# Kernel optimization log

Measured on AMD Instinct MI355X. Metric: run time of the kernel, lower is better.

Reference implementation:

```python
import jax, jax.numpy as jnp
import numpy as np

N_TP = 4  # number of heterogeneous agent types (experts)


def _mlp(x, w1, b1, w2, b2, w3, b3):
    h = jax.nn.relu(x @ w1 + b1)
    h = jax.nn.relu(h @ w2 + b2)
    return h @ w3 + b3


def setup_inputs() -> dict:
    key = jax.random.key(0)
    ks = jax.random.split(key, 12)
    T, A, D, H, NA = 2048, 128, 64, 64, 16
    s = 0.05
    return {
        "obs": jax.random.normal(ks[0], (T, A, D), dtype=jnp.float32),
        "hete_pick": jax.random.randint(ks[1], (T, A), 0, N_TP, dtype=jnp.int64),
        "gp_sel_summary": jax.random.uniform(ks[2], (T, N_TP), dtype=jnp.float32),
        "W1": jax.random.normal(ks[3], (N_TP, D + N_TP, H), dtype=jnp.float32) * s,
        "b1": jnp.zeros((N_TP, H), jnp.float32),
        "W2": jax.random.normal(ks[4], (N_TP, H, H), dtype=jnp.float32) * s,
        "b2": jnp.zeros((N_TP, H), jnp.float32),
        "W3": jax.random.normal(ks[5], (N_TP, H, NA), dtype=jnp.float32) * s,
        "b3": jnp.zeros((N_TP, NA), jnp.float32),
        "cW1": jax.random.normal(ks[6], (D + N_TP, H), dtype=jnp.float32) * s,
        "cb1": jnp.zeros((H,), jnp.float32),
        "cW2": jax.random.normal(ks[7], (H, H), dtype=jnp.float32) * s,
        "cb2": jnp.zeros((H,), jnp.float32),
        "cW3": jax.random.normal(ks[8], (H, 1), dtype=jnp.float32) * s,
        "cb3": jnp.zeros((1,), jnp.float32),
    }


def reference(obs, hete_pick, gp_sel_summary, W1, b1, W2, b2, W3, b3,
              cW1, cb1, cW2, cb2, cW3, cb3):
    T, A, D = obs.shape
    n_tp = W1.shape[0]
    # hete_info_obs: broadcast group-selection summary over agents, concat to obs
    hete_info = jnp.broadcast_to(gp_sel_summary[:, None, :], (T, A, n_tp))
    x = jnp.concatenate([obs, hete_info.astype(obs.dtype)], axis=-1)  # [T,A,D+n_tp]
    xf = x.reshape(T * A, D + n_tp)
    tp = hete_pick.reshape(T * A)
    # per-type dispatch: mask -> sub-net -> scatter back (expressed as masked select)
    logits = jnp.zeros((T * A, W3.shape[-1]), obs.dtype)
    for t in range(n_tp):
        out_t = _mlp(xf, W1[t], b1[t], W2[t], b2[t], W3[t], b3[t])
        logits = jnp.where((tp == t)[:, None], out_t, logits)
    # central critic runs on all agents
    value = _mlp(xf, cW1, cb1, cW2, cb2, cW3, cb3)  # [T*A,1]
    out = jnp.concatenate([logits, value], axis=-1)  # [T*A, n_action+1]
    return out.reshape(T, A, -1)
```

## Files before the change

kernel.cpp:

```cpp
#include <hip/hip_runtime.h>
#include <stdint.h>


typedef float v4f __attribute__((ext_vector_type(4)));
typedef short v8s __attribute__((ext_vector_type(8)));

#define NTOK   262144
#define XS_STR 104
#define HS_STR 136
#define WP2_OFF 30720
#define WP3_OFF 51200

static __device__ __forceinline__ short f2bf(float f) {
    union { float f; uint32_t u; } c; c.f = f;
    uint32_t u = c.u;
    uint32_t r = (u + 0x7FFFu + ((u >> 16) & 1u)) >> 16;
    return (short)r;
}


__global__ void count_kernel(const int* __restrict__ hete, int* __restrict__ hdr) {
    __shared__ int wc[4][4];
    int tid = threadIdx.x, lane = tid & 63, w = tid >> 6;
    int i = blockIdx.x * 256 + tid;
    int e = hete[i];
#pragma unroll
    for (int t = 0; t < 4; t++) {
        unsigned long long m = __ballot(e == t);
        if (lane == 0) wc[w][t] = __popcll(m);
    }
    __syncthreads();
    if (tid < 4) {
        int s = wc[0][tid] + wc[1][tid] + wc[2][tid] + wc[3][tid];
        atomicAdd(&hdr[tid], s);
    }
}

__global__ void prefix_kernel(int* __restrict__ hdr, int* __restrict__ bucket) {
    __shared__ int sa[5], sc[4];
    int tid = threadIdx.x;
    if (tid == 0) {
        int a = 0, ts = 0;
        for (int e = 0; e < 4; e++) {
            int c = hdr[e];
            sc[e] = c;
            sa[e] = a;
            hdr[4 + e]  = a;
            hdr[8 + e]  = a;
            hdr[13 + e] = ts;
            int tiles = (c + 127) >> 7;
            a  += tiles << 7;
            ts += tiles;
        }
        sa[4]   = a;
        hdr[12] = a;
        hdr[17] = ts;
    }
    __syncthreads();
    for (int e = 0; e < 4; e++) {
        int start = sa[e] + sc[e];
        int end   = sa[e + 1];
        for (int i = start + tid; i < end; i += 256) bucket[i] = -1;
    }
}

__global__ void scatter_kernel(const int* __restrict__ hete, int* __restrict__ hdr,
                               int* __restrict__ bucket) {
    __shared__ int wc[4][4], wb[4][4];
    int tid = threadIdx.x, lane = tid & 63, w = tid >> 6;
    int i = blockIdx.x * 256 + tid;
    int e = hete[i];
    unsigned long long lt = (1ull << lane) - 1ull;
    int rank = 0;
#pragma unroll
    for (int t = 0; t < 4; t++) {
        unsigned long long m = __ballot(e == t);
        if (lane == 0) wc[w][t] = __popcll(m);
        if (e == t) rank = __popcll(m & lt);
    }
    __syncthreads();
    if (tid < 4) {
        int t = tid, tot = 0;
#pragma unroll
        for (int ww = 0; ww < 4; ww++) tot += wc[ww][t];
        int base = atomicAdd(&hdr[4 + t], tot);
#pragma unroll
        for (int ww = 0; ww < 4; ww++) { int c = wc[ww][t]; wb[ww][t] = base; base += c; }
    }
    __syncthreads();
    bucket[wb[w][e] + rank] = i;
}


__global__ void prep_kernel(const float* __restrict__ W1, const float* __restrict__ cW1,
                            const float* __restrict__ W2, const float* __restrict__ cW2,
                            const float* __restrict__ W3, const float* __restrict__ cW3,
                            short* __restrict__ wp) {
    int b = blockIdx.x, lane = threadIdx.x;
    int nl = lane & 15, quad = lane >> 4;
    short frag[8];
    if (b < 60) {
        int e = b / 12, rem = b % 12, ks = rem / 4, nt = rem % 4;
        int n = nt * 16 + nl;
#pragma unroll
        for (int j = 0; j < 8; j++) {
            int k = ks * 32 + quad * 8 + j;
            float v = 0.f;
            if (k < 68) v = (e < 4) ? W1[(e * 68 + k) * 64 + n] : cW1[k * 64 + n];
            frag[j] = f2bf(v);
        }
    } else if (b < 100) {
        int u = b - 60, e = u / 8, ks = (u % 8) / 4, nt = u % 4;
        int n = nt * 16 + nl;
#pragma unroll
        for (int j = 0; j < 8; j++) {
            int k = ks * 32 + quad * 8 + j;
            frag[j] = f2bf((e < 4) ? W2[(e * 64 + k) * 64 + n] : cW2[k * 64 + n]);
        }
    } else {
        int u = b - 100;
#pragma unroll
        for (int j = 0; j < 8; j++) {
            int ks = (u < 8) ? (u & 1) : (u - 8);
            int k  = ks * 32 + quad * 8 + j;
            float v;
            if (u < 8) { int ee = u >> 1; v = W3[(ee * 64 + k) * 16 + nl]; }
            else       { v = (nl == 0) ? cW3[k] : 0.f; }
            frag[j] = f2bf(v);
        }
    }
    v8s pk = { frag[0], frag[1], frag[2], frag[3], frag[4], frag[5], frag[6], frag[7] };
    *(v8s*)(wp + (size_t)b * 512 + lane * 8) = pk;
}


__global__ __launch_bounds__(256) void main_kernel(
    const float* __restrict__ obs, const float* __restrict__ gp,
    const int* __restrict__ bucket, const int* __restrict__ hdr,
    const short* __restrict__ wp,
    const float* __restrict__ b1, const float* __restrict__ b2, const float* __restrict__ b3,
    const float* __restrict__ cb1, const float* __restrict__ cb2, const float* __restrict__ cb3,
    float* __restrict__ out)
{
    __shared__ __align__(16) short xs[128 * XS_STR];
    __shared__ __align__(16) short hs[128 * HS_STR];
    __shared__ int tokL[128];

    int b = blockIdx.x;
    int total = hdr[17];
    if (b >= total) return;
    int e = 3;
    if      (b < hdr[14]) e = 0;
    else if (b < hdr[15]) e = 1;
    else if (b < hdr[16]) e = 2;
    int slot0 = hdr[8 + e] + (b - hdr[13 + e]) * 128;

    int tid = threadIdx.x, lane = tid & 63, w = tid >> 6;
    int ml = lane & 15, quad = lane >> 4;

    if (tid < 128) tokL[tid] = bucket[slot0 + tid];

    {
        int r = tid >> 1, hh = tid & 1;
        int tk = bucket[slot0 + r];
        v8s z = { 0, 0, 0, 0, 0, 0, 0, 0 };
        if (tk >= 0) {
            const float4* src = (const float4*)(obs + (size_t)tk * 64 + hh * 32);
#pragma unroll
            for (int t = 0; t < 4; t++) {
                float4 f0 = src[2 * t], f1 = src[2 * t + 1];
                v8s pk = { f2bf(f0.x), f2bf(f0.y), f2bf(f0.z), f2bf(f0.w),
                           f2bf(f1.x), f2bf(f1.y), f2bf(f1.z), f2bf(f1.w) };
                *(v8s*)&xs[r * XS_STR + hh * 32 + t * 8] = pk;
            }
            if (hh) {
                const float* g = gp + (size_t)(tk >> 7) * 4;
                v8s pg = { f2bf(g[0]), f2bf(g[1]), f2bf(g[2]), f2bf(g[3]), 0, 0, 0, 0 };
                *(v8s*)&xs[r * XS_STR + 64] = pg;
                *(v8s*)&xs[r * XS_STR + 72] = z;
                *(v8s*)&xs[r * XS_STR + 80] = z;
                *(v8s*)&xs[r * XS_STR + 88] = z;
            }
        } else {
#pragma unroll
            for (int t = 0; t < 4; t++) *(v8s*)&xs[r * XS_STR + hh * 32 + t * 8] = z;
            if (hh) {
                *(v8s*)&xs[r * XS_STR + 64] = z;
                *(v8s*)&xs[r * XS_STR + 72] = z;
                *(v8s*)&xs[r * XS_STR + 80] = z;
                *(v8s*)&xs[r * XS_STR + 88] = z;
            }
        }
    }
    __syncthreads();

    v4f accE[8], accC[8];
#pragma unroll
    for (int m = 0; m < 8; m++) { accE[m] = (v4f){0,0,0,0}; accC[m] = (v4f){0,0,0,0}; }
#pragma unroll
    for (int ks = 0; ks < 3; ks++) {
        v8s bE = *(const v8s*)(wp + (size_t)((e * 3 + ks) * 4 + w) * 512 + lane * 8);
        v8s bC = *(const v8s*)(wp + (size_t)((12 + ks) * 4 + w) * 512 + lane * 8);
#pragma unroll
        for (int m = 0; m < 8; m++) {
            v8s a = *(const v8s*)&xs[(m * 16 + ml) * XS_STR + ks * 32 + quad * 8];
            accE[m] = __builtin_amdgcn_mfma_f32_16x16x32_bf16(a, bE, accE[m], 0, 0, 0);
            accC[m] = __builtin_amdgcn_mfma_f32_16x16x32_bf16(a, bC, accC[m], 0, 0, 0);
        }
    }
    {
        float bE1 = b1[e * 64 + w * 16 + ml], bC1 = cb1[w * 16 + ml];
#pragma unroll
        for (int m = 0; m < 8; m++)
#pragma unroll
            for (int rr = 0; rr < 4; rr++) {
                int row = m * 16 + quad * 4 + rr;
                hs[row * HS_STR + w * 16 + ml]      = f2bf(fmaxf(accE[m][rr] + bE1, 0.f));
                hs[row * HS_STR + 64 + w * 16 + ml] = f2bf(fmaxf(accC[m][rr] + bC1, 0.f));
            }
    }
    __syncthreads();

    v4f acc2E[8], acc2C[8];
#pragma unroll
    for (int m = 0; m < 8; m++) { acc2E[m] = (v4f){0,0,0,0}; acc2C[m] = (v4f){0,0,0,0}; }
#pragma unroll
    for (int ks = 0; ks < 2; ks++) {
        v8s bE = *(const v8s*)(wp + WP2_OFF + (size_t)((e * 2 + ks) * 4 + w) * 512 + lane * 8);
        v8s bC = *(const v8s*)(wp + WP2_OFF + (size_t)((8 + ks) * 4 + w) * 512 + lane * 8);
#pragma unroll
        for (int m = 0; m < 8; m++) {
            v8s aE = *(const v8s*)&hs[(m * 16 + ml) * HS_STR + ks * 32 + quad * 8];
            v8s aC = *(const v8s*)&hs[(m * 16 + ml) * HS_STR + 64 + ks * 32 + quad * 8];
            acc2E[m] = __builtin_amdgcn_mfma_f32_16x16x32_bf16(aE, bE, acc2E[m], 0, 0, 0);
            acc2C[m] = __builtin_amdgcn_mfma_f32_16x16x32_bf16(aC, bC, acc2C[m], 0, 0, 0);
        }
    }
    __syncthreads();
    {
        float bE2 = b2[e * 64 + w * 16 + ml], bC2 = cb2[w * 16 + ml];
#pragma unroll
        for (int m = 0; m < 8; m++)
#pragma unroll
            for (int rr = 0; rr < 4; rr++) {
                int row = m * 16 + quad * 4 + rr;
                hs[row * HS_STR + w * 16 + ml]      = f2bf(fmaxf(acc2E[m][rr] + bE2, 0.f));
                hs[row * HS_STR + 64 + w * 16 + ml] = f2bf(fmaxf(acc2C[m][rr] + bC2, 0.f));
            }
    }
    __syncthreads();

    v4f accL[2], accV[2];
#pragma unroll
    for (int mm = 0; mm < 2; mm++) { accL[mm] = (v4f){0,0,0,0}; accV[mm] = (v4f){0,0,0,0}; }
#pragma unroll
    for (int ks = 0; ks < 2; ks++) {
        v8s bW = *(const v8s*)(wp + WP3_OFF + (size_t)(e * 2 + ks) * 512 + lane * 8);
        v8s bV = *(const v8s*)(wp + WP3_OFF + (size_t)(8 + ks) * 512 + lane * 8);
#pragma unroll
        for (int mm = 0; mm < 2; mm++) {
            v8s aE = *(const v8s*)&hs[((2 * w + mm) * 16 + ml) * HS_STR + ks * 32 + quad * 8];
            v8s aC = *(const v8s*)&hs[((2 * w + mm) * 16 + ml) * HS_STR + 64 + ks * 32 + quad * 8];
            accL[mm] = __builtin_amdgcn_mfma_f32_16x16x32_bf16(aE, bW, accL[mm], 0, 0, 0);
            accV[mm] = __builtin_amdgcn_mfma_f32_16x16x32_bf16(aC, bV, accV[mm], 0, 0, 0);
        }
    }

    {
        float b3v = b3[e * 16 + ml], cb3v = cb3[0];
#pragma unroll
        for (int mm = 0; mm < 2; mm++)
#pragma unroll
            for (int rr = 0; rr < 4; rr++) {
                int row = (2 * w + mm) * 16 + quad * 4 + rr;
                int tk = tokL[row];
                if (tk >= 0) {
                    float* o = out + (size_t)tk * 17;
                    o[ml] = accL[mm][rr] + b3v;
                    if (ml == 0) o[16] = accV[mm][rr] + cb3v;
                }
            }
    }
}


extern "C" void kernel_launch(void* const* d_in, const int* in_sizes, int n_in,
                              void* d_out, int out_size, void* d_ws, size_t ws_size,
                              hipStream_t stream) {
    const float* obs = (const float*)d_in[0];
    const int*  hete = (const int*)d_in[1];
    const float* gp  = (const float*)d_in[2];
    const float* W1  = (const float*)d_in[3];
    const float* b1  = (const float*)d_in[4];
    const float* W2  = (const float*)d_in[5];
    const float* b2  = (const float*)d_in[6];
    const float* W3  = (const float*)d_in[7];
    const float* b3  = (const float*)d_in[8];
    const float* cW1 = (const float*)d_in[9];
    const float* cb1 = (const float*)d_in[10];
    const float* cW2 = (const float*)d_in[11];
    const float* cb2 = (const float*)d_in[12];
    const float* cW3 = (const float*)d_in[13];
    const float* cb3 = (const float*)d_in[14];
    float* out = (float*)d_out;

    int*   hdr    = (int*)d_ws;
    int*   bucket = hdr + 32;
    short* wp     = (short*)(bucket + 262656);

    hipMemsetAsync(hdr, 0, 128, stream);
    count_kernel  <<<1024, 256, 0, stream>>>(hete, hdr);
    prefix_kernel <<<1,    256, 0, stream>>>(hdr, bucket);
    scatter_kernel<<<1024, 256, 0, stream>>>(hete, hdr, bucket);
    prep_kernel   <<<110,   64, 0, stream>>>(W1, cW1, W2, cW2, W3, cW3, wp);
    main_kernel   <<<2051, 256, 0, stream>>>(obs, gp, bucket, hdr, wp,
                                             b1, b2, b3, cb1, cb2, cb3, out);
}
```

Baseline: 194.4 us.

## Replace bucketed expert dispatch with dense all-expert per-wave MLP evaluation

Removes the count, prefix and scatter kernels and the memset, and computes all four expert MLPs plus the critic for every token, selecting each token's logits by its type (the same masked-select form as the reference). Each wave owns 64 tokens, keeps its input fragments in registers, and uses a per-wave swizzled LDS buffer in place of block-wide shared tiles and barriers. The MFMA operand roles are swapped so that weights are the A operand, and occupancy is hinted through launch bounds. This trades about 2.5x more matrix work for removing the launch overhead of the sort kernels, the gather indirection and the block synchronisation.

```diff
diff --git a/kernel.cpp b/kernel.cpp
--- a/kernel.cpp
+++ b/kernel.cpp
@@ -5,9 +5,6 @@
 typedef float v4f __attribute__((ext_vector_type(4)));
 typedef short v8s __attribute__((ext_vector_type(8)));
 
-#define NTOK   262144
-#define XS_STR 104
-#define HS_STR 136
 #define WP2_OFF 30720
 #define WP3_OFF 51200
 
@@ -17,80 +14,9 @@
     uint32_t r = (u + 0x7FFFu + ((u >> 16) & 1u)) >> 16;
     return (short)r;
 }
-
-
-__global__ void count_kernel(const int* __restrict__ hete, int* __restrict__ hdr) {
-    __shared__ int wc[4][4];
-    int tid = threadIdx.x, lane = tid & 63, w = tid >> 6;
-    int i = blockIdx.x * 256 + tid;
-    int e = hete[i];
-#pragma unroll
-    for (int t = 0; t < 4; t++) {
-        unsigned long long m = __ballot(e == t);
-        if (lane == 0) wc[w][t] = __popcll(m);
-    }
-    __syncthreads();
-    if (tid < 4) {
-        int s = wc[0][tid] + wc[1][tid] + wc[2][tid] + wc[3][tid];
-        atomicAdd(&hdr[tid], s);
-    }
-}
-
-__global__ void prefix_kernel(int* __restrict__ hdr, int* __restrict__ bucket) {
-    __shared__ int sa[5], sc[4];
-    int tid = threadIdx.x;
-    if (tid == 0) {
-        int a = 0, ts = 0;
-        for (int e = 0; e < 4; e++) {
-            int c = hdr[e];
-            sc[e] = c;
-            sa[e] = a;
-            hdr[4 + e]  = a;
-            hdr[8 + e]  = a;
-            hdr[13 + e] = ts;
-            int tiles = (c + 127) >> 7;
-            a  += tiles << 7;
-            ts += tiles;
-        }
-        sa[4]   = a;
-        hdr[12] = a;
-        hdr[17] = ts;
-    }
-    __syncthreads();
-    for (int e = 0; e < 4; e++) {
-        int start = sa[e] + sc[e];
-        int end   = sa[e + 1];
-        for (int i = start + tid; i < end; i += 256) bucket[i] = -1;
-    }
-}
-
-__global__ void scatter_kernel(const int* __restrict__ hete, int* __restrict__ hdr,
-                               int* __restrict__ bucket) {
-    __shared__ int wc[4][4], wb[4][4];
-    int tid = threadIdx.x, lane = tid & 63, w = tid >> 6;
-    int i = blockIdx.x * 256 + tid;
-    int e = hete[i];
-    unsigned long long lt = (1ull << lane) - 1ull;
-    int rank = 0;
-#pragma unroll
-    for (int t = 0; t < 4; t++) {
-        unsigned long long m = __ballot(e == t);
-        if (lane == 0) wc[w][t] = __popcll(m);
-        if (e == t) rank = __popcll(m & lt);
-    }
-    __syncthreads();
-    if (tid < 4) {
-        int t = tid, tot = 0;
-#pragma unroll
-        for (int ww = 0; ww < 4; ww++) tot += wc[ww][t];
-        int base = atomicAdd(&hdr[4 + t], tot);
-#pragma unroll
-        for (int ww = 0; ww < 4; ww++) { int c = wc[ww][t]; wb[ww][t] = base; base += c; }
-    }
-    __syncthreads();
-    bucket[wb[w][e] + rank] = i;
-}
-
+static __device__ __forceinline__ uint32_t pk2(float a, float b) {
+    return (uint32_t)(uint16_t)f2bf(a) | ((uint32_t)(uint16_t)f2bf(b) << 16);
+}
 
 __global__ void prep_kernel(const float* __restrict__ W1, const float* __restrict__ cW1,
                             const float* __restrict__ W2, const float* __restrict__ cW2,
@@ -134,152 +60,158 @@
 }
 
 
-__global__ __launch_bounds__(256) void main_kernel(
+__global__ __launch_bounds__(256, 3) void main_kernel(
     const float* __restrict__ obs, const float* __restrict__ gp,
-    const int* __restrict__ bucket, const int* __restrict__ hdr,
-    const short* __restrict__ wp,
+    const int* __restrict__ hete, const short* __restrict__ wp,
     const float* __restrict__ b1, const float* __restrict__ b2, const float* __restrict__ b3,
     const float* __restrict__ cb1, const float* __restrict__ cb2, const float* __restrict__ cb3,
     float* __restrict__ out)
 {
-    __shared__ __align__(16) short xs[128 * XS_STR];
-    __shared__ __align__(16) short hs[128 * HS_STR];
-    __shared__ int tokL[128];
-
-    int b = blockIdx.x;
-    int total = hdr[17];
-    if (b >= total) return;
-    int e = 3;
-    if      (b < hdr[14]) e = 0;
-    else if (b < hdr[15]) e = 1;
-    else if (b < hdr[16]) e = 2;
-    int slot0 = hdr[8 + e] + (b - hdr[13 + e]) * 128;
-
-    int tid = threadIdx.x, lane = tid & 63, w = tid >> 6;
+    __shared__ __align__(16) uint32_t H_[4][64 * 36];
+    int tid = threadIdx.x, wv = tid >> 6, lane = tid & 63;
     int ml = lane & 15, quad = lane >> 4;
-
-    if (tid < 128) tokL[tid] = bucket[slot0 + tid];
-
-    {
-        int r = tid >> 1, hh = tid & 1;
-        int tk = bucket[slot0 + r];
-        v8s z = { 0, 0, 0, 0, 0, 0, 0, 0 };
-        if (tk >= 0) {
-            const float4* src = (const float4*)(obs + (size_t)tk * 64 + hh * 32);
-#pragma unroll
-            for (int t = 0; t < 4; t++) {
-                float4 f0 = src[2 * t], f1 = src[2 * t + 1];
-                v8s pk = { f2bf(f0.x), f2bf(f0.y), f2bf(f0.z), f2bf(f0.w),
-                           f2bf(f1.x), f2bf(f1.y), f2bf(f1.z), f2bf(f1.w) };
-                *(v8s*)&xs[r * XS_STR + hh * 32 + t * 8] = pk;
-            }
-            if (hh) {
-                const float* g = gp + (size_t)(tk >> 7) * 4;
-                v8s pg = { f2bf(g[0]), f2bf(g[1]), f2bf(g[2]), f2bf(g[3]), 0, 0, 0, 0 };
-                *(v8s*)&xs[r * XS_STR + 64] = pg;
-                *(v8s*)&xs[r * XS_STR + 72] = z;
-                *(v8s*)&xs[r * XS_STR + 80] = z;
-                *(v8s*)&xs[r * XS_STR + 88] = z;
-            }
-        } else {
-#pragma unroll
-            for (int t = 0; t < 4; t++) *(v8s*)&xs[r * XS_STR + hh * 32 + t * 8] = z;
-            if (hh) {
-                *(v8s*)&xs[r * XS_STR + 64] = z;
-                *(v8s*)&xs[r * XS_STR + 72] = z;
-                *(v8s*)&xs[r * XS_STR + 80] = z;
-                *(v8s*)&xs[r * XS_STR + 88] = z;
-            }
-        }
-    }
-    __syncthreads();
-
-    v4f accE[8], accC[8];
-#pragma unroll
-    for (int m = 0; m < 8; m++) { accE[m] = (v4f){0,0,0,0}; accC[m] = (v4f){0,0,0,0}; }
-#pragma unroll
-    for (int ks = 0; ks < 3; ks++) {
-        v8s bE = *(const v8s*)(wp + (size_t)((e * 3 + ks) * 4 + w) * 512 + lane * 8);
-        v8s bC = *(const v8s*)(wp + (size_t)((12 + ks) * 4 + w) * 512 + lane * 8);
-#pragma unroll
-        for (int m = 0; m < 8; m++) {
-            v8s a = *(const v8s*)&xs[(m * 16 + ml) * XS_STR + ks * 32 + quad * 8];
-            accE[m] = __builtin_amdgcn_mfma_f32_16x16x32_bf16(a, bE, accE[m], 0, 0, 0);
-            accC[m] = __builtin_amdgcn_mfma_f32_16x16x32_bf16(a, bC, accC[m], 0, 0, 0);
-        }
-    }
-    {
-        float bE1 = b1[e * 64 + w * 16 + ml], bC1 = cb1[w * 16 + ml];
-#pragma unroll
-        for (int m = 0; m < 8; m++)
-#pragma unroll
-            for (int rr = 0; rr < 4; rr++) {
-                int row = m * 16 + quad * 4 + rr;
-                hs[row * HS_STR + w * 16 + ml]      = f2bf(fmaxf(accE[m][rr] + bE1, 0.f));
-                hs[row * HS_STR + 64 + w * 16 + ml] = f2bf(fmaxf(accC[m][rr] + bC1, 0.f));
-            }
-    }
-    __syncthreads();
-
-    v4f acc2E[8], acc2C[8];
-#pragma unroll
-    for (int m = 0; m < 8; m++) { acc2E[m] = (v4f){0,0,0,0}; acc2C[m] = (v4f){0,0,0,0}; }
-#pragma unroll
-    for (int ks = 0; ks < 2; ks++) {
-        v8s bE = *(const v8s*)(wp + WP2_OFF + (size_t)((e * 2 + ks) * 4 + w) * 512 + lane * 8);
-        v8s bC = *(const v8s*)(wp + WP2_OFF + (size_t)((8 + ks) * 4 + w) * 512 + lane * 8);
-#pragma unroll
-        for (int m = 0; m < 8; m++) {
-            v8s aE = *(const v8s*)&hs[(m * 16 + ml) * HS_STR + ks * 32 + quad * 8];
-            v8s aC = *(const v8s*)&hs[(m * 16 + ml) * HS_STR + 64 + ks * 32 + quad * 8];
-            acc2E[m] = __builtin_amdgcn_mfma_f32_16x16x32_bf16(aE, bE, acc2E[m], 0, 0, 0);
-            acc2C[m] = __builtin_amdgcn_mfma_f32_16x16x32_bf16(aC, bC, acc2C[m], 0, 0, 0);
-        }
-    }
-    __syncthreads();
-    {
-        float bE2 = b2[e * 64 + w * 16 + ml], bC2 = cb2[w * 16 + ml];
-#pragma unroll
-        for (int m = 0; m < 8; m++)
-#pragma unroll
-            for (int rr = 0; rr < 4; rr++) {
-                int row = m * 16 + quad * 4 + rr;
-                hs[row * HS_STR + w * 16 + ml]      = f2bf(fmaxf(acc2E[m][rr] + bE2, 0.f));
-                hs[row * HS_STR + 64 + w * 16 + ml] = f2bf(fmaxf(acc2C[m][rr] + bC2, 0.f));
-            }
-    }
-    __syncthreads();
-
-    v4f accL[2], accV[2];
-#pragma unroll
-    for (int mm = 0; mm < 2; mm++) { accL[mm] = (v4f){0,0,0,0}; accV[mm] = (v4f){0,0,0,0}; }
-#pragma unroll
-    for (int ks = 0; ks < 2; ks++) {
-        v8s bW = *(const v8s*)(wp + WP3_OFF + (size_t)(e * 2 + ks) * 512 + lane * 8);
-        v8s bV = *(const v8s*)(wp + WP3_OFF + (size_t)(8 + ks) * 512 + lane * 8);
-#pragma unroll
-        for (int mm = 0; mm < 2; mm++) {
-            v8s aE = *(const v8s*)&hs[((2 * w + mm) * 16 + ml) * HS_STR + ks * 32 + quad * 8];
-            v8s aC = *(const v8s*)&hs[((2 * w + mm) * 16 + ml) * HS_STR + 64 + ks * 32 + quad * 8];
-            accL[mm] = __builtin_amdgcn_mfma_f32_16x16x32_bf16(aE, bW, accL[mm], 0, 0, 0);
-            accV[mm] = __builtin_amdgcn_mfma_f32_16x16x32_bf16(aC, bV, accV[mm], 0, 0, 0);
-        }
-    }
-
-    {
-        float b3v = b3[e * 16 + ml], cb3v = cb3[0];
-#pragma unroll
-        for (int mm = 0; mm < 2; mm++)
-#pragma unroll
-            for (int rr = 0; rr < 4; rr++) {
-                int row = (2 * w + mm) * 16 + quad * 4 + rr;
-                int tk = tokL[row];
-                if (tk >= 0) {
-                    float* o = out + (size_t)tk * 17;
-                    o[ml] = accL[mm][rr] + b3v;
-                    if (ml == 0) o[16] = accV[mm][rr] + cb3v;
+    uint32_t* H = H_[wv];
+    int base = (blockIdx.x * 4 + wv) * 64;
+
+    v8s      xf[2][4];
+    uint32_t gpk[4][2];
+    int      tpv[4];
+    float    oE[4][4];
+    float    oV[4];
+
+#pragma unroll
+    for (int tt = 0; tt < 4; tt++) {
+        int tok = base + tt * 16 + ml;
+        tpv[tt] = hete[tok];
+        const float* xr = obs + (size_t)tok * 64 + quad * 8;
+#pragma unroll
+        for (int ks = 0; ks < 2; ks++) {
+            float4 a = *(const float4*)(xr + ks * 32);
+            float4 c = *(const float4*)(xr + ks * 32 + 4);
+            v8s f;
+            f[0] = f2bf(a.x); f[1] = f2bf(a.y); f[2] = f2bf(a.z); f[3] = f2bf(a.w);
+            f[4] = f2bf(c.x); f[5] = f2bf(c.y); f[6] = f2bf(c.z); f[7] = f2bf(c.w);
+            xf[ks][tt] = f;
+        }
+        if (quad == 0) {
+            float4 g = *(const float4*)(gp + (size_t)(tok >> 7) * 4);
+            gpk[tt][0] = pk2(g.x, g.y); gpk[tt][1] = pk2(g.z, g.w);
+        } else { gpk[tt][0] = 0; gpk[tt][1] = 0; }
+    }
+
+    float cb3v = cb3[0];
+
+    for (int ne = 0; ne < 5; ne++) {
+        v4f acc[4][4];
+#pragma unroll
+        for (int tt = 0; tt < 4; tt++)
+#pragma unroll
+            for (int nt = 0; nt < 4; nt++) acc[tt][nt] = (v4f){0.f, 0.f, 0.f, 0.f};
+#pragma unroll
+        for (int ks = 0; ks < 3; ks++) {
+            v8s wa[4];
+#pragma unroll
+            for (int nt = 0; nt < 4; nt++)
+                wa[nt] = *(const v8s*)(wp + (size_t)((ne * 3 + ks) * 4 + nt) * 512 + lane * 8);
+#pragma unroll
+            for (int tt = 0; tt < 4; tt++) {
+                v8s xb;
+                if (ks < 2) xb = xf[ks][tt];
+                else {
+                    union { uint32_t u[4]; v8s s; } cv;
+                    cv.u[0] = gpk[tt][0]; cv.u[1] = gpk[tt][1]; cv.u[2] = 0; cv.u[3] = 0;
+                    xb = cv.s;
                 }
-            }
+#pragma unroll
+                for (int nt = 0; nt < 4; nt++)
+                    acc[tt][nt] = __builtin_amdgcn_mfma_f32_16x16x32_bf16(wa[nt], xb, acc[tt][nt], 0, 0, 0);
+            }
+        }
+        const float* B1 = (ne < 4) ? (b1 + ne * 64) : cb1;
+        float4 bv[4];
+#pragma unroll
+        for (int nt = 0; nt < 4; nt++) bv[nt] = *(const float4*)(B1 + nt * 16 + quad * 4);
+#pragma unroll
+        for (int tt = 0; tt < 4; tt++) {
+            int tL = tt * 16 + ml, rb = tL * 36, sw = tL & 7;
+#pragma unroll
+            for (int nt = 0; nt < 4; nt++) {
+                float v0 = fmaxf(acc[tt][nt][0] + bv[nt].x, 0.f);
+                float v1 = fmaxf(acc[tt][nt][1] + bv[nt].y, 0.f);
+                float v2 = fmaxf(acc[tt][nt][2] + bv[nt].z, 0.f);
+                float v3 = fmaxf(acc[tt][nt][3] + bv[nt].w, 0.f);
+                int g = 2 * nt + (quad >> 1);
+                uint2 w2 = { pk2(v0, v1), pk2(v2, v3) };
+                *(uint2*)&H[rb + ((g ^ sw) << 2) + 2 * (quad & 1)] = w2;
+            }
+        }
+        v8s wa2[2][4];
+#pragma unroll
+        for (int ks2 = 0; ks2 < 2; ks2++)
+#pragma unroll
+            for (int nt = 0; nt < 4; nt++)
+                wa2[ks2][nt] = *(const v8s*)(wp + WP2_OFF +
+                    (size_t)((ne * 2 + ks2) * 4 + nt) * 512 + lane * 8);
+        const float* B2 = (ne < 4) ? (b2 + ne * 64) : cb2;
+        float4 bv2[4];
+#pragma unroll
+        for (int nt = 0; nt < 4; nt++) bv2[nt] = *(const float4*)(B2 + nt * 16 + quad * 4);
+        v8s w3f[2];
+#pragma unroll
+        for (int ks2 = 0; ks2 < 2; ks2++)
+            w3f[ks2] = *(const v8s*)(wp + WP3_OFF +
+                (size_t)((ne < 4) ? (ne * 2 + ks2) : (8 + ks2)) * 512 + lane * 8);
+        float4 b3v = (ne < 4) ? *(const float4*)(b3 + ne * 16 + quad * 4)
+                              : (float4){0.f, 0.f, 0.f, 0.f};
+
+#pragma unroll
+        for (int tt = 0; tt < 4; tt++) {
+            int tL = tt * 16 + ml, rb = tL * 36, sw = tL & 7;
+            v4f a2[4];
+#pragma unroll
+            for (int nt = 0; nt < 4; nt++) a2[nt] = (v4f){0.f, 0.f, 0.f, 0.f};
+#pragma unroll
+            for (int ks2 = 0; ks2 < 2; ks2++) {
+                v8s hf = *(const v8s*)&H[rb + (((4 * ks2 + quad) ^ sw) << 2)];
+#pragma unroll
+                for (int nt = 0; nt < 4; nt++)
+                    a2[nt] = __builtin_amdgcn_mfma_f32_16x16x32_bf16(wa2[ks2][nt], hf, a2[nt], 0, 0, 0);
+            }
+#pragma unroll
+            for (int nt = 0; nt < 4; nt++) {
+                float v0 = fmaxf(a2[nt][0] + bv2[nt].x, 0.f);
+                float v1 = fmaxf(a2[nt][1] + bv2[nt].y, 0.f);
+                float v2 = fmaxf(a2[nt][2] + bv2[nt].z, 0.f);
+                float v3 = fmaxf(a2[nt][3] + bv2[nt].w, 0.f);
+                int g = 2 * nt + (quad >> 1);
+                uint2 w2 = { pk2(v0, v1), pk2(v2, v3) };
+                *(uint2*)&H[rb + ((g ^ sw) << 2) + 2 * (quad & 1)] = w2;
+            }
+            v4f a3 = (v4f){0.f, 0.f, 0.f, 0.f};
+#pragma unroll
+            for (int ks2 = 0; ks2 < 2; ks2++) {
+                v8s hf2 = *(const v8s*)&H[rb + (((4 * ks2 + quad) ^ sw) << 2)];
+                a3 = __builtin_amdgcn_mfma_f32_16x16x32_bf16(w3f[ks2], hf2, a3, 0, 0, 0);
+            }
+            if (ne < 4) {
+#pragma unroll
+                for (int rr = 0; rr < 4; rr++) {
+                    float val = a3[rr] + ((const float*)&b3v)[rr];
+                    if (tpv[tt] == ne) oE[tt][rr] = val;
+                }
+            } else {
+                oV[tt] = a3[0] + cb3v;
+            }
+        }
+    }
+
+#pragma unroll
+    for (int tt = 0; tt < 4; tt++) {
+        int tok = base + tt * 16 + ml;
+        float* o = out + (size_t)tok * 17 + quad * 4;
+#pragma unroll
+        for (int rr = 0; rr < 4; rr++) o[rr] = oE[tt][rr];
+        if (quad == 0) out[(size_t)tok * 17 + 16] = oV[tt];
     }
 }
 
@@ -304,15 +236,9 @@
     const float* cb3 = (const float*)d_in[14];
     float* out = (float*)d_out;
 
-    int*   hdr    = (int*)d_ws;
-    int*   bucket = hdr + 32;
-    short* wp     = (short*)(bucket + 262656);
-
-    hipMemsetAsync(hdr, 0, 128, stream);
-    count_kernel  <<<1024, 256, 0, stream>>>(hete, hdr);
-    prefix_kernel <<<1,    256, 0, stream>>>(hdr, bucket);
-    scatter_kernel<<<1024, 256, 0, stream>>>(hete, hdr, bucket);
-    prep_kernel   <<<110,   64, 0, stream>>>(W1, cW1, W2, cW2, W3, cW3, wp);
-    main_kernel   <<<2051, 256, 0, stream>>>(obs, gp, bucket, hdr, wp,
-                                             b1, b2, b3, cb1, cb2, cb3, out);
-}
+    short* wp = (short*)d_ws;
+
+    prep_kernel<<<110,   64, 0, stream>>>(W1, cW1, W2, cW2, W3, cW3, wp);
+    main_kernel<<<1024, 256, 0, stream>>>(obs, gp, hete, wp,
+                                          b1, b2, b3, cb1, cb2, cb3, out);
+}
```

Result: no change. 192.9 us (-0.7%).
